# Performance work log

Hardware: AMD Instinct MI355X
Metric: run time of the kernel (lower is better)

## Reference

```python
import jax, jax.numpy as jnp
import numpy as np

H, W = 32, 32
DIM = 768
NUM_BLOCKS = 4
BLOCK = DIM // NUM_BLOCKS
SCALE = 0.02


def setup_inputs() -> dict:
    key = jax.random.key(0)
    k0, k1, k2, k3, k4 = jax.random.split(key, 5)
    B, N, C = 64, H * W, DIM
    x = jax.random.normal(k0, (B, N, C), dtype=jnp.float32)
    w1 = SCALE * jax.random.normal(k1, (2, NUM_BLOCKS, BLOCK, BLOCK), dtype=jnp.float32)
    b1 = SCALE * jax.random.normal(k2, (2, NUM_BLOCKS, BLOCK), dtype=jnp.float32)
    w2 = SCALE * jax.random.normal(k3, (2, NUM_BLOCKS, BLOCK, BLOCK), dtype=jnp.float32)
    b2 = SCALE * jax.random.normal(k4, (2, NUM_BLOCKS, BLOCK), dtype=jnp.float32)
    return {"x": x, "w1": w1, "b1": b1, "w2": w2, "b2": b2}


def _mul(inp, weights):
    # inp: [B, H, Wf, blocks, d], weights: [blocks, d, k]
    return jnp.einsum('...bd,bdk->...bk', inp, weights)


def reference(x, w1, b1, w2, b2):
    B, N, C = x.shape
    xg = x.reshape(B, H, W, C)
    xf = jnp.fft.rfft2(xg, axes=(1, 2), norm='ortho')  # [B, H, W//2+1, C] complex64
    xf = xf.reshape(B, xf.shape[1], xf.shape[2], NUM_BLOCKS, BLOCK)
    xr, xi = xf.real, xf.imag
    # layer 1: complex block-diagonal linear + ReLU
    r1 = jax.nn.relu(_mul(xr, w1[0]) - _mul(xi, w1[1]) + b1[0])
    i1 = jax.nn.relu(_mul(xr, w1[1]) + _mul(xi, w1[0]) + b1[1])
    # layer 2 (faithful to original: imag uses the already-updated real part)
    r2 = _mul(r1, w2[0]) - _mul(i1, w2[1]) + b2[0]
    i2 = _mul(r2, w2[1]) + _mul(i1, w2[0]) + b2[1]
    xc = (r2 + 1j * i2).reshape(B, r2.shape[1], r2.shape[2], C)
    out = jnp.fft.irfft2(xc, s=(H, W), axes=(1, 2), norm='ortho')
    return out.reshape(B, N, C) + jnp.zeros_like(x)  # bias is zeros (self.bias is None)
```

## Files before the change

### kernel.cpp

```cpp
#include <hip/hip_runtime.h>
#include <cstddef>
#include <cstdint>


typedef __attribute__((ext_vector_type(8))) short bf16x8;
typedef __attribute__((ext_vector_type(4))) float f32x4;

namespace {

constexpr int BATCH = 64;
constexpr int Hh    = 32;
constexpr int Ww    = 32;
constexpr int WF    = 17;
constexpr int CC    = 768;
constexpr int BLK   = 192;

constexpr size_t W_ELEMS  = 16u * 36864u;
constexpr size_t TW_ELEMS = 4u * 1024u;
constexpr size_t PW_ELEMS = W_ELEMS + TW_ELEMS;
constexpr size_t SPEC_ELEMS = (size_t)BATCH * WF * Hh * CC;

constexpr float C32[32] = {
   1.0000000000f,  0.9807852804f,  0.9238795325f,  0.8314696123f,
   0.7071067812f,  0.5555702330f,  0.3826834324f,  0.1950903220f,
   0.0000000000f, -0.1950903220f, -0.3826834324f, -0.5555702330f,
  -0.7071067812f, -0.8314696123f, -0.9238795325f, -0.9807852804f,
  -1.0000000000f, -0.9807852804f, -0.9238795325f, -0.8314696123f,
  -0.7071067812f, -0.5555702330f, -0.3826834324f, -0.1950903220f,
   0.0000000000f,  0.1950903220f,  0.3826834324f,  0.5555702330f,
   0.7071067812f,  0.8314696123f,  0.9238795325f,  0.9807852804f
};
constexpr float S32[32] = {
   0.0000000000f,  0.1950903220f,  0.3826834324f,  0.5555702330f,
   0.7071067812f,  0.8314696123f,  0.9238795325f,  0.9807852804f,
   1.0000000000f,  0.9807852804f,  0.9238795325f,  0.8314696123f,
   0.7071067812f,  0.5555702330f,  0.3826834324f,  0.1950903220f,
   0.0000000000f, -0.1950903220f, -0.3826834324f, -0.5555702330f,
  -0.7071067812f, -0.8314696123f, -0.9238795325f, -0.9807852804f,
  -1.0000000000f, -0.9807852804f, -0.9238795325f, -0.8314696123f,
  -0.7071067812f, -0.5555702330f, -0.3826834324f, -0.1950903220f
};

}

__device__ __forceinline__ ushort f2bf(float f) {
    union { float f; unsigned u; } v; v.f = f;
    const unsigned r = (v.u + 0x7FFFu + ((v.u >> 16) & 1u)) >> 16;
    return (ushort)r;
}
__device__ __forceinline__ float bf2f(ushort u) {
    union { unsigned u; float f; } v; v.u = ((unsigned)u) << 16;
    return v.f;
}
__device__ __forceinline__ bf16x8 neg8(bf16x8 a) {
    union { bf16x8 v; uint4 u; } t; t.v = a;
    t.u.x ^= 0x80008000u; t.u.y ^= 0x80008000u;
    t.u.z ^= 0x80008000u; t.u.w ^= 0x80008000u;
    return t.v;
}

__global__ __launch_bounds__(256) void k_pack(const float* __restrict__ w1,
                                              const float* __restrict__ w2,
                                              ushort* __restrict__ pw) {
    const unsigned idx = blockIdx.x * 256u + threadIdx.x;
    if (idx < W_ELEMS) {
        const unsigned mi = idx / 36864u;
        const unsigned r  = idx % 36864u;
        const unsigned kk = r / 6144u;
        const unsigned r2 = r % 6144u;
        const unsigned nf = r2 / 512u;
        const unsigned r3 = r2 % 512u;
        const unsigned lane = r3 / 8u;
        const unsigned i  = r3 % 8u;
        const unsigned d   = kk * 32u + (lane >> 4) * 8u + i;
        const unsigned col = nf * 16u + (lane & 15u);
        const unsigned which = mi >> 2, blk = mi & 3u;
        const float* src = (which < 2u)
            ? (w1 + (size_t)(which * 4u + blk) * BLK * BLK)
            : (w2 + (size_t)((which - 2u) * 4u + blk) * BLK * BLK);
        pw[idx] = f2bf(src[(size_t)d * BLK + col]);
    } else {
        const unsigned t = idx - (unsigned)W_ELEMS;
        const unsigned mat = t >> 10;
        const unsigned rr  = t & 1023u;
        const unsigned mf  = rr >> 9;
        const unsigned q   = rr & 511u;
        const unsigned lane = q >> 3, i = q & 7u;
        const unsigned row = mf * 16u + (lane & 15u);
        const unsigned col = (lane >> 4) * 8u + i;
        const unsigned ang = (row * col) & 31u;
        float v;
        if      (mat == 0u) v = C32[ang] * 0.03125f;
        else if (mat == 1u) v = S32[ang] * 0.03125f;
        else if (mat == 2u) v = C32[ang];
        else                v = S32[ang];
        pw[idx] = f2bf(v);
    }
}

__global__ __launch_bounds__(256) void k_rfft_w(const float* __restrict__ x,
                                                ushort* __restrict__ sRe,
                                                ushort* __restrict__ sIm) {
    const int bid = blockIdx.x;
    const int bh  = bid / 3;
    const int c   = (bid % 3) * 256 + threadIdx.x;

    const float* px = x + (size_t)bh * Ww * CC + c;
    float v[32];
#pragma unroll
    for (int w = 0; w < 32; ++w) v[w] = px[(size_t)w * CC];

    float av[16], bv[16];
#pragma unroll
    for (int w = 1; w <= 15; ++w) { av[w] = v[w] + v[32 - w]; bv[w] = v[w] - v[32 - w]; }

    const int b = bh >> 5, h = bh & 31;
    const size_t ob = ((size_t)b * WF * Hh + h) * CC + c;
#pragma unroll
    for (int k = 0; k <= 16; ++k) {
        float sr = v[0] + ((k & 1) ? -v[16] : v[16]);
        float si = 0.f;
#pragma unroll
        for (int w = 1; w <= 15; ++w) {
            const int t = (k * w) & 31;
            sr = fmaf(av[w],  C32[t], sr);
            si = fmaf(bv[w], -S32[t], si);
        }
        sRe[ob + (size_t)k * Hh * CC] = f2bf(sr);
        sIm[ob + (size_t)k * Hh * CC] = f2bf(si);
    }
}

__device__ __forceinline__ bf16x8 gatherB(const ushort* pl, int col, int lg) {
    union { bf16x8 v; ushort u[8]; } t;
#pragma unroll
    for (int i = 0; i < 8; ++i) t.u[i] = pl[(lg * 8 + i) * 200 + col];
    return t.v;
}

__global__ __launch_bounds__(256) void k_fft_mix(
        ushort* __restrict__ sRe, ushort* __restrict__ sIm,
        const ushort* __restrict__ pw,
        const float* __restrict__ b1, const float* __restrict__ b2) {

    __shared__ ushort lds[6][32][200];

    const int bid = blockIdx.x;
    const int blk = bid / (BATCH * WF);
    const int rem = bid % (BATCH * WF);
    const int b   = rem / WF;
    const int kw  = rem % WF;
    const int tid = threadIdx.x;
    const int wv = tid >> 6, l = tid & 63, lc = l & 15, lg = l >> 4;

    const size_t gbase = ((size_t)b * WF + kw) * Hh * CC + blk * BLK;

#pragma unroll
    for (int j = 0; j < 3; ++j) {
        const int q = tid + 256 * j;
        const int h = q / 24, c8 = (q % 24) * 8;
        const uint4 vr = *(const uint4*)(sRe + gbase + (size_t)h * CC + c8);
        const uint4 vi = *(const uint4*)(sIm + gbase + (size_t)h * CC + c8);
        *(uint4*)&lds[0][h][c8] = vr;
        *(uint4*)&lds[1][h][c8] = vi;
    }
    __syncthreads();

    const ushort* TW = pw + W_ELEMS;
    const int col0 = wv * 48;

    {
        bf16x8 cf[2], sf[2], sfn[2];
#pragma unroll
        for (int m = 0; m < 2; ++m) {
            cf[m]  = *(const bf16x8*)(TW + ((size_t)(0 * 2 + m) * 64 + l) * 8);
            sf[m]  = *(const bf16x8*)(TW + ((size_t)(1 * 2 + m) * 64 + l) * 8);
            sfn[m] = neg8(sf[m]);
        }
        bf16x8 xr[3], xi[3];
#pragma unroll
        for (int n = 0; n < 3; ++n) {
            xr[n] = gatherB(&lds[0][0][0], col0 + n * 16 + lc, lg);
            xi[n] = gatherB(&lds[1][0][0], col0 + n * 16 + lc, lg);
        }
        f32x4 yr[2][3] = {}, yi[2][3] = {};
#pragma unroll
        for (int m = 0; m < 2; ++m)
#pragma unroll
            for (int n = 0; n < 3; ++n) {
                yr[m][n] = __builtin_amdgcn_mfma_f32_16x16x32_bf16(cf[m],  xr[n], yr[m][n], 0, 0, 0);
                yr[m][n] = __builtin_amdgcn_mfma_f32_16x16x32_bf16(sf[m],  xi[n], yr[m][n], 0, 0, 0);
                yi[m][n] = __builtin_amdgcn_mfma_f32_16x16x32_bf16(cf[m],  xi[n], yi[m][n], 0, 0, 0);
                yi[m][n] = __builtin_amdgcn_mfma_f32_16x16x32_bf16(sfn[m], xr[n], yi[m][n], 0, 0, 0);
            }
#pragma unroll
        for (int m = 0; m < 2; ++m)
#pragma unroll
            for (int n = 0; n < 3; ++n)
#pragma unroll
                for (int r = 0; r < 4; ++r) {
                    lds[2][m * 16 + lg * 4 + r][col0 + n * 16 + lc] = f2bf(yr[m][n][r]);
                    lds[3][m * 16 + lg * 4 + r][col0 + n * 16 + lc] = f2bf(yi[m][n][r]);
                }
    }
    __syncthreads();

    const ushort* pW1r = pw + (size_t)(0 * 4 + blk) * 36864;
    const ushort* pW1i = pw + (size_t)(1 * 4 + blk) * 36864;
    const ushort* pW2r = pw + (size_t)(2 * 4 + blk) * 36864;
    const ushort* pW2i = pw + (size_t)(3 * 4 + blk) * 36864;

    {
        f32x4 aR[2][3], aI[2][3];
#pragma unroll
        for (int n = 0; n < 3; ++n) {
            const float br = b1[(size_t)(0 * 4 + blk) * BLK + col0 + n * 16 + lc];
            const float bi = b1[(size_t)(1 * 4 + blk) * BLK + col0 + n * 16 + lc];
#pragma unroll
            for (int m = 0; m < 2; ++m) {
                aR[m][n] = (f32x4){br, br, br, br};
                aI[m][n] = (f32x4){bi, bi, bi, bi};
            }
        }
#pragma unroll
        for (int kk = 0; kk < 6; ++kk) {
            bf16x8 ar[2], ai[2], ain[2];
#pragma unroll
            for (int m = 0; m < 2; ++m) {
                ar[m]  = *(const bf16x8*)&lds[2][m * 16 + lc][kk * 32 + lg * 8];
                ai[m]  = *(const bf16x8*)&lds[3][m * 16 + lc][kk * 32 + lg * 8];
                ain[m] = neg8(ai[m]);
            }
            bf16x8 wr[3], wi[3];
#pragma unroll
            for (int n = 0; n < 3; ++n) {
                const size_t off = ((size_t)(kk * 12 + wv * 3 + n) * 64 + l) * 8;
                wr[n] = *(const bf16x8*)(pW1r + off);
                wi[n] = *(const bf16x8*)(pW1i + off);
            }
#pragma unroll
            for (int m = 0; m < 2; ++m)
#pragma unroll
                for (int n = 0; n < 3; ++n) {
                    aR[m][n] = __builtin_amdgcn_mfma_f32_16x16x32_bf16(ar[m],  wr[n], aR[m][n], 0, 0, 0);
                    aR[m][n] = __builtin_amdgcn_mfma_f32_16x16x32_bf16(ain[m], wi[n], aR[m][n], 0, 0, 0);
                    aI[m][n] = __builtin_amdgcn_mfma_f32_16x16x32_bf16(ar[m],  wi[n], aI[m][n], 0, 0, 0);
                    aI[m][n] = __builtin_amdgcn_mfma_f32_16x16x32_bf16(ai[m],  wr[n], aI[m][n], 0, 0, 0);
                }
        }
#pragma unroll
        for (int m = 0; m < 2; ++m)
#pragma unroll
            for (int n = 0; n < 3; ++n)
#pragma unroll
                for (int r = 0; r < 4; ++r) {
                    float rv = aR[m][n][r]; rv = rv > 0.f ? rv : 0.f;
                    float iv = aI[m][n][r]; iv = iv > 0.f ? iv : 0.f;
                    lds[4][m * 16 + lg * 4 + r][col0 + n * 16 + lc] = f2bf(rv);
                    lds[5][m * 16 + lg * 4 + r][col0 + n * 16 + lc] = f2bf(iv);
                }
    }
    __syncthreads();

    {
        f32x4 cR[2][3];
#pragma unroll
        for (int n = 0; n < 3; ++n) {
            const float br = b2[(size_t)(0 * 4 + blk) * BLK + col0 + n * 16 + lc];
#pragma unroll
            for (int m = 0; m < 2; ++m) cR[m][n] = (f32x4){br, br, br, br};
        }
#pragma unroll
        for (int kk = 0; kk < 6; ++kk) {
            bf16x8 ar[2], ain[2];
#pragma unroll
            for (int m = 0; m < 2; ++m) {
                ar[m]  = *(const bf16x8*)&lds[4][m * 16 + lc][kk * 32 + lg * 8];
                ain[m] = neg8(*(const bf16x8*)&lds[5][m * 16 + lc][kk * 32 + lg * 8]);
            }
            bf16x8 wr[3], wi[3];
#pragma unroll
            for (int n = 0; n < 3; ++n) {
                const size_t off = ((size_t)(kk * 12 + wv * 3 + n) * 64 + l) * 8;
                wr[n] = *(const bf16x8*)(pW2r + off);
                wi[n] = *(const bf16x8*)(pW2i + off);
            }
#pragma unroll
            for (int m = 0; m < 2; ++m)
#pragma unroll
                for (int n = 0; n < 3; ++n) {
                    cR[m][n] = __builtin_amdgcn_mfma_f32_16x16x32_bf16(ar[m],  wr[n], cR[m][n], 0, 0, 0);
                    cR[m][n] = __builtin_amdgcn_mfma_f32_16x16x32_bf16(ain[m], wi[n], cR[m][n], 0, 0, 0);
                }
        }
#pragma unroll
        for (int m = 0; m < 2; ++m)
#pragma unroll
            for (int n = 0; n < 3; ++n)
#pragma unroll
                for (int r = 0; r < 4; ++r)
                    lds[0][m * 16 + lg * 4 + r][col0 + n * 16 + lc] = f2bf(cR[m][n][r]);
    }
    __syncthreads();

    {
        f32x4 cI[2][3];
#pragma unroll
        for (int n = 0; n < 3; ++n) {
            const float bi = b2[(size_t)(1 * 4 + blk) * BLK + col0 + n * 16 + lc];
#pragma unroll
            for (int m = 0; m < 2; ++m) cI[m][n] = (f32x4){bi, bi, bi, bi};
        }
#pragma unroll
        for (int kk = 0; kk < 6; ++kk) {
            bf16x8 a2[2], i1[2];
#pragma unroll
            for (int m = 0; m < 2; ++m) {
                a2[m] = *(const bf16x8*)&lds[0][m * 16 + lc][kk * 32 + lg * 8];
                i1[m] = *(const bf16x8*)&lds[5][m * 16 + lc][kk * 32 + lg * 8];
            }
            bf16x8 wr[3], wi[3];
#pragma unroll
            for (int n = 0; n < 3; ++n) {
                const size_t off = ((size_t)(kk * 12 + wv * 3 + n) * 64 + l) * 8;
                wr[n] = *(const bf16x8*)(pW2r + off);
                wi[n] = *(const bf16x8*)(pW2i + off);
            }
#pragma unroll
            for (int m = 0; m < 2; ++m)
#pragma unroll
                for (int n = 0; n < 3; ++n) {
                    cI[m][n] = __builtin_amdgcn_mfma_f32_16x16x32_bf16(a2[m], wi[n], cI[m][n], 0, 0, 0);
                    cI[m][n] = __builtin_amdgcn_mfma_f32_16x16x32_bf16(i1[m], wr[n], cI[m][n], 0, 0, 0);
                }
        }
#pragma unroll
        for (int m = 0; m < 2; ++m)
#pragma unroll
            for (int n = 0; n < 3; ++n)
#pragma unroll
                for (int r = 0; r < 4; ++r)
                    lds[1][m * 16 + lg * 4 + r][col0 + n * 16 + lc] = f2bf(cI[m][n][r]);
    }
    __syncthreads();

    {
        bf16x8 ci[2], si[2], sin_[2];
#pragma unroll
        for (int m = 0; m < 2; ++m) {
            ci[m]   = *(const bf16x8*)(TW + ((size_t)(2 * 2 + m) * 64 + l) * 8);
            si[m]   = *(const bf16x8*)(TW + ((size_t)(3 * 2 + m) * 64 + l) * 8);
            sin_[m] = neg8(si[m]);
        }
        bf16x8 r2b[3], i2b[3];
#pragma unroll
        for (int n = 0; n < 3; ++n) {
            r2b[n] = gatherB(&lds[0][0][0], col0 + n * 16 + lc, lg);
            i2b[n] = gatherB(&lds[1][0][0], col0 + n * 16 + lc, lg);
        }
        f32x4 zr[2][3] = {}, zi[2][3] = {};
#pragma unroll
        for (int m = 0; m < 2; ++m)
#pragma unroll
            for (int n = 0; n < 3; ++n) {
                zr[m][n] = __builtin_amdgcn_mfma_f32_16x16x32_bf16(ci[m],   r2b[n], zr[m][n], 0, 0, 0);
                zr[m][n] = __builtin_amdgcn_mfma_f32_16x16x32_bf16(sin_[m], i2b[n], zr[m][n], 0, 0, 0);
                zi[m][n] = __builtin_amdgcn_mfma_f32_16x16x32_bf16(ci[m],   i2b[n], zi[m][n], 0, 0, 0);
                zi[m][n] = __builtin_amdgcn_mfma_f32_16x16x32_bf16(si[m],   r2b[n], zi[m][n], 0, 0, 0);
            }
#pragma unroll
        for (int m = 0; m < 2; ++m)
#pragma unroll
            for (int n = 0; n < 3; ++n)
#pragma unroll
                for (int r = 0; r < 4; ++r) {
                    const int row = m * 16 + lg * 4 + r;
                    const size_t g = gbase + (size_t)row * CC + col0 + n * 16 + lc;
                    sRe[g] = f2bf(zr[m][n][r]);
                    sIm[g] = f2bf(zi[m][n][r]);
                }
    }
}

__global__ __launch_bounds__(256) void k_irfft_w(const ushort* __restrict__ sRe,
                                                 const ushort* __restrict__ sIm,
                                                 float* __restrict__ out) {
    const int bid = blockIdx.x;
    const int bh  = bid / 3;
    const int c   = (bid % 3) * 256 + threadIdx.x;
    const int b = bh >> 5, h = bh & 31;

    const size_t ib = ((size_t)b * WF * Hh + h) * CC + c;
    float xr[17], xi[17];
#pragma unroll
    for (int k = 0; k < 17; ++k) {
        xr[k] = bf2f(sRe[ib + (size_t)k * Hh * CC]);
        xi[k] = bf2f(sIm[ib + (size_t)k * Hh * CC]);
    }
    float* po = out + (size_t)bh * Ww * CC + c;
#pragma unroll
    for (int w = 0; w <= 16; ++w) {
        float e = xr[0] + ((w & 1) ? -xr[16] : xr[16]);
        float o = 0.f;
#pragma unroll
        for (int k = 1; k <= 15; ++k) {
            const int t = (k * w) & 31;
            e = fmaf(2.f * xr[k],  C32[t], e);
            o = fmaf(2.f * xi[k], -S32[t], o);
        }
        po[(size_t)w * CC] = (e + o) * 0.03125f;
        if (w >= 1 && w <= 15)
            po[(size_t)(32 - w) * CC] = (e - o) * 0.03125f;
    }
}

extern "C" void kernel_launch(void* const* d_in, const int* in_sizes, int n_in,
                              void* d_out, int out_size, void* d_ws, size_t ws_size,
                              hipStream_t stream) {
    const float* x  = (const float*)d_in[0];
    const float* w1 = (const float*)d_in[1];
    const float* b1 = (const float*)d_in[2];
    const float* w2 = (const float*)d_in[3];
    const float* b2 = (const float*)d_in[4];
    float* out = (float*)d_out;

    ushort* pw   = (ushort*)d_ws;
    ushort* sRe  = pw + PW_ELEMS;
    ushort* sIm  = sRe + SPEC_ELEMS;

    k_pack<<<dim3((unsigned)(PW_ELEMS / 256)), dim3(256), 0, stream>>>(w1, w2, pw);
    k_rfft_w<<<dim3(BATCH * Hh * 3), dim3(256), 0, stream>>>(x, sRe, sIm);
    k_fft_mix<<<dim3(4 * BATCH * WF), dim3(256), 0, stream>>>(sRe, sIm, pw, b1, b2);
    k_irfft_w<<<dim3(BATCH * Hh * 3), dim3(256), 0, stream>>>(sRe, sIm, out);
}
```

Measured before the change: 254.6 us.

## Repack spectrum into swizzled h-pair interleaved layout and shrink mix LDS

The intermediate spectrum is stored in a new layout. Pairs of h rows are interleaved into 32-bit words, grouped into 16-column sub-tiles with an XOR swizzle, and real and imaginary planes sit next to each other. The row FFT and inverse FFT kernels now each handle two h rows per thread and issue packed 32-bit stores and loads. The mix kernel loads contiguous tiles and replaces the 8-way strided LDS gathers with 4 dword reads. It also reuses LDS buffers, cutting 6 planes to 4, and sets launch_bounds to 3 blocks per CU for occupancy. This adds an extra barrier and more complex indexing, and doubles per-thread register pressure in the FFT kernels.

```diff
diff --git a/kernel.cpp b/kernel.cpp
--- a/kernel.cpp
+++ b/kernel.cpp
@@ -18,7 +18,9 @@
 constexpr size_t W_ELEMS  = 16u * 36864u;
 constexpr size_t TW_ELEMS = 4u * 1024u;
 constexpr size_t PW_ELEMS = W_ELEMS + TW_ELEMS;
-constexpr size_t SPEC_ELEMS = (size_t)BATCH * WF * Hh * CC;
+
+constexpr int PLANE_U = 48 * 512;
+constexpr size_t SPEC_ELEMS = (size_t)BATCH * WF * 2 * PLANE_U;
 
 constexpr float C32[32] = {
    1.0000000000f,  0.9807852804f,  0.9238795325f,  0.8314696123f,
@@ -79,7 +81,7 @@
             ? (w1 + (size_t)(which * 4u + blk) * BLK * BLK)
             : (w2 + (size_t)((which - 2u) * 4u + blk) * BLK * BLK);
         pw[idx] = f2bf(src[(size_t)d * BLK + col]);
-    } else {
+    } else if (idx < PW_ELEMS) {
         const unsigned t = idx - (unsigned)W_ELEMS;
         const unsigned mat = t >> 10;
         const unsigned rr  = t & 1023u;
@@ -99,51 +101,54 @@
 }
 
 __global__ __launch_bounds__(256) void k_rfft_w(const float* __restrict__ x,
-                                                ushort* __restrict__ sRe,
-                                                ushort* __restrict__ sIm) {
+                                                ushort* __restrict__ spec) {
     const int bid = blockIdx.x;
-    const int bh  = bid / 3;
-    const int c   = (bid % 3) * 256 + threadIdx.x;
-
-    const float* px = x + (size_t)bh * Ww * CC + c;
-    float v[32];
-#pragma unroll
-    for (int w = 0; w < 32; ++w) v[w] = px[(size_t)w * CC];
-
-    float av[16], bv[16];
-#pragma unroll
-    for (int w = 1; w <= 15; ++w) { av[w] = v[w] + v[32 - w]; bv[w] = v[w] - v[32 - w]; }
-
-    const int b = bh >> 5, h = bh & 31;
-    const size_t ob = ((size_t)b * WF * Hh + h) * CC + c;
+    const int cc = bid % 3;
+    const int hp = (bid / 3) & 15;
+    const int b  = bid / 48;
+    const int c  = cc * 256 + threadIdx.x;
+
+    uint pr[17], pi[17];
+    const float* p0 = x + ((size_t)b * 1024 + hp * 64) * CC + c;
+#pragma unroll
+    for (int half = 0; half < 2; ++half) {
+        const float* px = p0 + (size_t)half * 32 * CC;
+        float v[32];
+#pragma unroll
+        for (int w = 0; w < 32; ++w) v[w] = px[(size_t)w * CC];
+        float av[16], bv[16];
+#pragma unroll
+        for (int w = 1; w <= 15; ++w) { av[w] = v[w] + v[32 - w]; bv[w] = v[w] - v[32 - w]; }
+#pragma unroll
+        for (int k = 0; k <= 16; ++k) {
+            float sr = v[0] + ((k & 1) ? -v[16] : v[16]);
+            float si = 0.f;
+#pragma unroll
+            for (int w = 1; w <= 15; ++w) {
+                const int t = (k * w) & 31;
+                sr = fmaf(av[w],  C32[t], sr);
+                si = fmaf(bv[w], -S32[t], si);
+            }
+            if (half == 0) { pr[k] = f2bf(sr); pi[k] = f2bf(si); }
+            else { pr[k] |= (uint)f2bf(sr) << 16; pi[k] |= (uint)f2bf(si) << 16; }
+        }
+    }
+    const size_t base = (size_t)b * (WF * 2 * PLANE_U)
+                      + (size_t)(c >> 4) * 512 + hp * 32
+                      + (((c & 15) ^ ((hp & 7) << 1)) << 1);
 #pragma unroll
     for (int k = 0; k <= 16; ++k) {
-        float sr = v[0] + ((k & 1) ? -v[16] : v[16]);
-        float si = 0.f;
-#pragma unroll
-        for (int w = 1; w <= 15; ++w) {
-            const int t = (k * w) & 31;
-            sr = fmaf(av[w],  C32[t], sr);
-            si = fmaf(bv[w], -S32[t], si);
-        }
-        sRe[ob + (size_t)k * Hh * CC] = f2bf(sr);
-        sIm[ob + (size_t)k * Hh * CC] = f2bf(si);
-    }
-}
-
-__device__ __forceinline__ bf16x8 gatherB(const ushort* pl, int col, int lg) {
-    union { bf16x8 v; ushort u[8]; } t;
-#pragma unroll
-    for (int i = 0; i < 8; ++i) t.u[i] = pl[(lg * 8 + i) * 200 + col];
-    return t.v;
-}
-
-__global__ __launch_bounds__(256) void k_fft_mix(
-        ushort* __restrict__ sRe, ushort* __restrict__ sIm,
+        *(uint*)(spec + base + (size_t)k * (2 * PLANE_U)) = pr[k];
+        *(uint*)(spec + base + (size_t)k * (2 * PLANE_U) + PLANE_U) = pi[k];
+    }
+}
+
+__global__ __launch_bounds__(256, 3) void k_fft_mix(
+        ushort* __restrict__ spec,
         const ushort* __restrict__ pw,
         const float* __restrict__ b1, const float* __restrict__ b2) {
 
-    __shared__ ushort lds[6][32][200];
+    __shared__ ushort lds[4][6336];
 
     const int bid = blockIdx.x;
     const int blk = bid / (BATCH * WF);
@@ -153,16 +158,15 @@
     const int tid = threadIdx.x;
     const int wv = tid >> 6, l = tid & 63, lc = l & 15, lg = l >> 4;
 
-    const size_t gbase = ((size_t)b * WF + kw) * Hh * CC + blk * BLK;
+    const size_t gR = ((size_t)(b * WF + kw) * 2) * PLANE_U + blk * 6144;
+    const size_t gI = gR + PLANE_U;
 
 #pragma unroll
     for (int j = 0; j < 3; ++j) {
         const int q = tid + 256 * j;
-        const int h = q / 24, c8 = (q % 24) * 8;
-        const uint4 vr = *(const uint4*)(sRe + gbase + (size_t)h * CC + c8);
-        const uint4 vi = *(const uint4*)(sIm + gbase + (size_t)h * CC + c8);
-        *(uint4*)&lds[0][h][c8] = vr;
-        *(uint4*)&lds[1][h][c8] = vi;
+        const int dst = (q >> 6) * 528 + (q & 63) * 8;
+        *(uint4*)&lds[0][dst] = *(const uint4*)(spec + gR + q * 8);
+        *(uint4*)&lds[1][dst] = *(const uint4*)(spec + gI + q * 8);
     }
     __syncthreads();
 
@@ -170,6 +174,20 @@
     const int col0 = wv * 48;
 
     {
+        bf16x8 xr[3], xi[3];
+#pragma unroll
+        for (int n = 0; n < 3; ++n) {
+            const int csub = wv * 3 + n;
+            union { bf16x8 v; uint d[4]; } ur, ui;
+#pragma unroll
+            for (int t = 0; t < 4; ++t) {
+                const int hp = lg * 4 + t;
+                const int pos = csub * 528 + hp * 32 + ((lc ^ ((hp & 7) << 1)) << 1);
+                ur.d[t] = *(const uint*)&lds[0][pos];
+                ui.d[t] = *(const uint*)&lds[1][pos];
+            }
+            xr[n] = ur.v; xi[n] = ui.v;
+        }
         bf16x8 cf[2], sf[2], sfn[2];
 #pragma unroll
         for (int m = 0; m < 2; ++m) {
@@ -177,12 +195,6 @@
             sf[m]  = *(const bf16x8*)(TW + ((size_t)(1 * 2 + m) * 64 + l) * 8);
             sfn[m] = neg8(sf[m]);
         }
-        bf16x8 xr[3], xi[3];
-#pragma unroll
-        for (int n = 0; n < 3; ++n) {
-            xr[n] = gatherB(&lds[0][0][0], col0 + n * 16 + lc, lg);
-            xi[n] = gatherB(&lds[1][0][0], col0 + n * 16 + lc, lg);
-        }
         f32x4 yr[2][3] = {}, yi[2][3] = {};
 #pragma unroll
         for (int m = 0; m < 2; ++m)
@@ -199,8 +211,9 @@
             for (int n = 0; n < 3; ++n)
 #pragma unroll
                 for (int r = 0; r < 4; ++r) {
-                    lds[2][m * 16 + lg * 4 + r][col0 + n * 16 + lc] = f2bf(yr[m][n][r]);
-                    lds[3][m * 16 + lg * 4 + r][col0 + n * 16 + lc] = f2bf(yi[m][n][r]);
+                    const int pos = (wv * 3 + n) * 528 + (m * 16 + lg * 4 + r) * 16 + lc;
+                    lds[0][pos] = f2bf(yr[m][n][r]);
+                    lds[1][pos] = f2bf(yi[m][n][r]);
                 }
     }
     __syncthreads();
@@ -224,11 +237,13 @@
         }
 #pragma unroll
         for (int kk = 0; kk < 6; ++kk) {
+            const int csubA = 2 * kk + (lg >> 1);
+            const int apos  = csubA * 528 + lc * 16 + (lg & 1) * 8;
             bf16x8 ar[2], ai[2], ain[2];
 #pragma unroll
             for (int m = 0; m < 2; ++m) {
-                ar[m]  = *(const bf16x8*)&lds[2][m * 16 + lc][kk * 32 + lg * 8];
-                ai[m]  = *(const bf16x8*)&lds[3][m * 16 + lc][kk * 32 + lg * 8];
+                ar[m]  = *(const bf16x8*)&lds[0][apos + m * 256];
+                ai[m]  = *(const bf16x8*)&lds[1][apos + m * 256];
                 ain[m] = neg8(ai[m]);
             }
             bf16x8 wr[3], wi[3];
@@ -248,6 +263,7 @@
                     aI[m][n] = __builtin_amdgcn_mfma_f32_16x16x32_bf16(ai[m],  wr[n], aI[m][n], 0, 0, 0);
                 }
         }
+        __syncthreads();
 #pragma unroll
         for (int m = 0; m < 2; ++m)
 #pragma unroll
@@ -256,8 +272,9 @@
                 for (int r = 0; r < 4; ++r) {
                     float rv = aR[m][n][r]; rv = rv > 0.f ? rv : 0.f;
                     float iv = aI[m][n][r]; iv = iv > 0.f ? iv : 0.f;
-                    lds[4][m * 16 + lg * 4 + r][col0 + n * 16 + lc] = f2bf(rv);
-                    lds[5][m * 16 + lg * 4 + r][col0 + n * 16 + lc] = f2bf(iv);
+                    const int pos = (wv * 3 + n) * 528 + (m * 16 + lg * 4 + r) * 16 + lc;
+                    lds[2][pos] = f2bf(rv);
+                    lds[3][pos] = f2bf(iv);
                 }
     }
     __syncthreads();
@@ -272,11 +289,13 @@
         }
 #pragma unroll
         for (int kk = 0; kk < 6; ++kk) {
+            const int csubA = 2 * kk + (lg >> 1);
+            const int apos  = csubA * 528 + lc * 16 + (lg & 1) * 8;
             bf16x8 ar[2], ain[2];
 #pragma unroll
             for (int m = 0; m < 2; ++m) {
-                ar[m]  = *(const bf16x8*)&lds[4][m * 16 + lc][kk * 32 + lg * 8];
-                ain[m] = neg8(*(const bf16x8*)&lds[5][m * 16 + lc][kk * 32 + lg * 8]);
+                ar[m]  = *(const bf16x8*)&lds[2][apos + m * 256];
+                ain[m] = neg8(*(const bf16x8*)&lds[3][apos + m * 256]);
             }
             bf16x8 wr[3], wi[3];
 #pragma unroll
@@ -296,15 +315,25 @@
 #pragma unroll
         for (int m = 0; m < 2; ++m)
 #pragma unroll
-            for (int n = 0; n < 3; ++n)
-#pragma unroll
-                for (int r = 0; r < 4; ++r)
-                    lds[0][m * 16 + lg * 4 + r][col0 + n * 16 + lc] = f2bf(cR[m][n][r]);
+            for (int n = 0; n < 3; ++n) {
+                const int csub = wv * 3 + n;
+#pragma unroll
+                for (int rp = 0; rp < 2; ++rp) {
+                    const ushort lo = f2bf(cR[m][n][2 * rp]);
+                    const ushort hi = f2bf(cR[m][n][2 * rp + 1]);
+                    const int kh0 = m * 16 + lg * 4 + 2 * rp;
+                    lds[0][csub * 528 + kh0 * 16 + lc]       = lo;
+                    lds[0][csub * 528 + (kh0 + 1) * 16 + lc] = hi;
+                    const int hp = kh0 >> 1;
+                    const int post = csub * 528 + hp * 32 + ((lc ^ ((hp & 7) << 1)) << 1);
+                    *(uint*)&lds[1][post] = (uint)lo | ((uint)hi << 16);
+                }
+            }
     }
     __syncthreads();
 
+    f32x4 cI[2][3];
     {
-        f32x4 cI[2][3];
 #pragma unroll
         for (int n = 0; n < 3; ++n) {
             const float bi = b2[(size_t)(1 * 4 + blk) * BLK + col0 + n * 16 + lc];
@@ -313,11 +342,13 @@
         }
 #pragma unroll
         for (int kk = 0; kk < 6; ++kk) {
+            const int csubA = 2 * kk + (lg >> 1);
+            const int apos  = csubA * 528 + lc * 16 + (lg & 1) * 8;
             bf16x8 a2[2], i1[2];
 #pragma unroll
             for (int m = 0; m < 2; ++m) {
-                a2[m] = *(const bf16x8*)&lds[0][m * 16 + lc][kk * 32 + lg * 8];
-                i1[m] = *(const bf16x8*)&lds[5][m * 16 + lc][kk * 32 + lg * 8];
+                a2[m] = *(const bf16x8*)&lds[0][apos + m * 256];
+                i1[m] = *(const bf16x8*)&lds[3][apos + m * 256];
             }
             bf16x8 wr[3], wi[3];
 #pragma unroll
@@ -337,12 +368,17 @@
 #pragma unroll
         for (int m = 0; m < 2; ++m)
 #pragma unroll
-            for (int n = 0; n < 3; ++n)
-#pragma unroll
-                for (int r = 0; r < 4; ++r)
-                    lds[1][m * 16 + lg * 4 + r][col0 + n * 16 + lc] = f2bf(cI[m][n][r]);
-    }
-    __syncthreads();
+            for (int n = 0; n < 3; ++n) {
+                const int csub = wv * 3 + n;
+#pragma unroll
+                for (int rp = 0; rp < 2; ++rp) {
+                    const int hp = (m * 16 + lg * 4 + 2 * rp) >> 1;
+                    const int post = csub * 528 + hp * 32 + ((lc ^ ((hp & 7) << 1)) << 1);
+                    *(uint*)&lds[2][post] =
+                        (uint)f2bf(cI[m][n][2 * rp]) | ((uint)f2bf(cI[m][n][2 * rp + 1]) << 16);
+                }
+            }
+    }
 
     {
         bf16x8 ci[2], si[2], sin_[2];
@@ -355,8 +391,16 @@
         bf16x8 r2b[3], i2b[3];
 #pragma unroll
         for (int n = 0; n < 3; ++n) {
-            r2b[n] = gatherB(&lds[0][0][0], col0 + n * 16 + lc, lg);
-            i2b[n] = gatherB(&lds[1][0][0], col0 + n * 16 + lc, lg);
+            const int csub = wv * 3 + n;
+            union { bf16x8 v; uint d[4]; } ur, ui;
+#pragma unroll
+            for (int t = 0; t < 4; ++t) {
+                const int hp = lg * 4 + t;
+                const int pos = csub * 528 + hp * 32 + ((lc ^ ((hp & 7) << 1)) << 1);
+                ur.d[t] = *(const uint*)&lds[1][pos];
+                ui.d[t] = *(const uint*)&lds[2][pos];
+            }
+            r2b[n] = ur.v; i2b[n] = ui.v;
         }
         f32x4 zr[2][3] = {}, zi[2][3] = {};
 #pragma unroll
@@ -371,46 +415,61 @@
 #pragma unroll
         for (int m = 0; m < 2; ++m)
 #pragma unroll
-            for (int n = 0; n < 3; ++n)
-#pragma unroll
-                for (int r = 0; r < 4; ++r) {
-                    const int row = m * 16 + lg * 4 + r;
-                    const size_t g = gbase + (size_t)row * CC + col0 + n * 16 + lc;
-                    sRe[g] = f2bf(zr[m][n][r]);
-                    sIm[g] = f2bf(zi[m][n][r]);
-                }
-    }
-}
-
-__global__ __launch_bounds__(256) void k_irfft_w(const ushort* __restrict__ sRe,
-                                                 const ushort* __restrict__ sIm,
+            for (int n = 0; n < 3; ++n) {
+                const size_t cbase = gR + (size_t)(wv * 3 + n) * 512;
+#pragma unroll
+                for (int rp = 0; rp < 2; ++rp) {
+                    const int hp = (m * 16 + lg * 4 + 2 * rp) >> 1;
+                    const size_t pos = cbase + hp * 32 + ((lc ^ ((hp & 7) << 1)) << 1);
+                    *(uint*)(spec + pos) =
+                        (uint)f2bf(zr[m][n][2 * rp]) | ((uint)f2bf(zr[m][n][2 * rp + 1]) << 16);
+                    *(uint*)(spec + pos + PLANE_U) =
+                        (uint)f2bf(zi[m][n][2 * rp]) | ((uint)f2bf(zi[m][n][2 * rp + 1]) << 16);
+                }
+            }
+    }
+}
+
+__global__ __launch_bounds__(256) void k_irfft_w(const ushort* __restrict__ spec,
                                                  float* __restrict__ out) {
     const int bid = blockIdx.x;
-    const int bh  = bid / 3;
-    const int c   = (bid % 3) * 256 + threadIdx.x;
-    const int b = bh >> 5, h = bh & 31;
-
-    const size_t ib = ((size_t)b * WF * Hh + h) * CC + c;
-    float xr[17], xi[17];
-#pragma unroll
-    for (int k = 0; k < 17; ++k) {
-        xr[k] = bf2f(sRe[ib + (size_t)k * Hh * CC]);
-        xi[k] = bf2f(sIm[ib + (size_t)k * Hh * CC]);
-    }
-    float* po = out + (size_t)bh * Ww * CC + c;
+    const int cc = bid % 3;
+    const int hp = (bid / 3) & 15;
+    const int b  = bid / 48;
+    const int c  = cc * 256 + threadIdx.x;
+
+    const size_t base = (size_t)b * (WF * 2 * PLANE_U)
+                      + (size_t)(c >> 4) * 512 + hp * 32
+                      + (((c & 15) ^ ((hp & 7) << 1)) << 1);
+    float xr0[17], xi0[17], xr1[17], xi1[17];
+#pragma unroll
+    for (int k = 0; k <= 16; ++k) {
+        const uint ur = *(const uint*)(spec + base + (size_t)k * (2 * PLANE_U));
+        const uint ui = *(const uint*)(spec + base + (size_t)k * (2 * PLANE_U) + PLANE_U);
+        xr0[k] = bf2f((ushort)ur); xr1[k] = bf2f((ushort)(ur >> 16));
+        xi0[k] = bf2f((ushort)ui); xi1[k] = bf2f((ushort)(ui >> 16));
+    }
+    float* po0 = out + ((size_t)b * 1024 + hp * 64) * CC + c;
+    float* po1 = po0 + (size_t)32 * CC;
 #pragma unroll
     for (int w = 0; w <= 16; ++w) {
-        float e = xr[0] + ((w & 1) ? -xr[16] : xr[16]);
-        float o = 0.f;
+        float e0 = xr0[0] + ((w & 1) ? -xr0[16] : xr0[16]);
+        float e1 = xr1[0] + ((w & 1) ? -xr1[16] : xr1[16]);
+        float o0 = 0.f, o1 = 0.f;
 #pragma unroll
         for (int k = 1; k <= 15; ++k) {
             const int t = (k * w) & 31;
-            e = fmaf(2.f * xr[k],  C32[t], e);
-            o = fmaf(2.f * xi[k], -S32[t], o);
-        }
-        po[(size_t)w * CC] = (e + o) * 0.03125f;
-        if (w >= 1 && w <= 15)
-            po[(size_t)(32 - w) * CC] = (e - o) * 0.03125f;
+            e0 = fmaf(2.f * xr0[k],  C32[t], e0);
+            o0 = fmaf(2.f * xi0[k], -S32[t], o0);
+            e1 = fmaf(2.f * xr1[k],  C32[t], e1);
+            o1 = fmaf(2.f * xi1[k], -S32[t], o1);
+        }
+        po0[(size_t)w * CC] = (e0 + o0) * 0.03125f;
+        po1[(size_t)w * CC] = (e1 + o1) * 0.03125f;
+        if (w >= 1 && w <= 15) {
+            po0[(size_t)(32 - w) * CC] = (e0 - o0) * 0.03125f;
+            po1[(size_t)(32 - w) * CC] = (e1 - o1) * 0.03125f;
+        }
     }
 }
 
@@ -425,11 +484,10 @@
     float* out = (float*)d_out;
 
     ushort* pw   = (ushort*)d_ws;
-    ushort* sRe  = pw + PW_ELEMS;
-    ushort* sIm  = sRe + SPEC_ELEMS;
-
-    k_pack<<<dim3((unsigned)(PW_ELEMS / 256)), dim3(256), 0, stream>>>(w1, w2, pw);
-    k_rfft_w<<<dim3(BATCH * Hh * 3), dim3(256), 0, stream>>>(x, sRe, sIm);
-    k_fft_mix<<<dim3(4 * BATCH * WF), dim3(256), 0, stream>>>(sRe, sIm, pw, b1, b2);
-    k_irfft_w<<<dim3(BATCH * Hh * 3), dim3(256), 0, stream>>>(sRe, sIm, out);
-}
+    ushort* spec = pw + PW_ELEMS;
+
+    k_pack<<<dim3((unsigned)((PW_ELEMS + 255) / 256)), dim3(256), 0, stream>>>(w1, w2, pw);
+    k_rfft_w<<<dim3(BATCH * 16 * 3), dim3(256), 0, stream>>>(x, spec);
+    k_fft_mix<<<dim3(4 * BATCH * WF), dim3(256), 0, stream>>>(spec, pw, b1, b2);
+    k_irfft_w<<<dim3(BATCH * 16 * 3), dim3(256), 0, stream>>>(spec, out);
+}
```

New measurement: 253.2 us. About the same (-0.5%).
